# Performance work log

Hardware: AMD Instinct MI355X
Metric: run time of the kernel (lower is better)

Reference implementation:

```python
import jax, jax.numpy as jnp
import numpy as np


def setup_inputs() -> dict:
    key = jax.random.key(0)
    k1, k2, k3, k4, k5 = jax.random.split(key, 5)
    T, R, K, D = 8, 512, 4, 4096          # tiles, rows/tile, group size, in_features
    N_CW = 16384                           # codebook size
    N_TOK = 512                            # tokens
    x = jax.random.normal(k1, (N_TOK, D), dtype=jnp.float32)
    codewords = jax.random.normal(k2, (N_CW, D), dtype=jnp.float32) * 0.02
    indices = jax.random.randint(k3, (T, R, K), 0, N_CW, dtype=jnp.int64)
    rotations = jax.random.normal(k4, (T, D, D), dtype=jnp.float32) * (1.0 / np.sqrt(D))
    scales = jax.random.uniform(k5, (T,), dtype=jnp.float32) + 0.5
    bias = jnp.zeros((D,), dtype=jnp.float32)
    return {"x": x, "codewords": codewords, "indices": indices,
            "rotations": rotations, "scales": scales, "bias": bias}


def reference(x, codewords, indices, rotations, scales, bias):
    # Decode weight tiles: gather [T,R,K,D] -> mean over group -> [T,R,D]
    decoded = codewords[indices].mean(axis=2)
    # Per-tile rotation and scale: [T,R,D] @ [T,D,D] -> [T,R,D]
    decoded = jnp.einsum('trd,tde->tre', decoded, rotations) * scales[:, None, None]
    T, R, D = decoded.shape
    weight = decoded.reshape(T * R, D)     # [out_features, in_features]
    # Linear: x @ W^T + b
    return x @ weight.T + bias
```

## Files before the change

### kernel.cpp

```cpp
#include <hip/hip_runtime.h>

typedef unsigned int uint32;
typedef unsigned short u16;
typedef float fx4 __attribute__((ext_vector_type(4)));
typedef uint32 u32x4 __attribute__((ext_vector_type(4)));

typedef const __attribute__((address_space(1))) void gvoid;
typedef __attribute__((address_space(3))) void lvoid;

#define MFMA_BF16_16x16x32(acc, a, b) \
  asm("v_mfma_f32_16x16x32_bf16 %0, %1, %2, %0" : "+v"(acc) : "v"(a), "v"(b))

#define WAIT_LGKM0() asm volatile("s_waitcnt lgkmcnt(0)" ::: "memory")
#define WAIT_LGKM4() asm volatile("s_waitcnt lgkmcnt(4)" ::: "memory")
#define WAIT_VM0()   asm volatile("s_waitcnt vmcnt(0)" ::: "memory")
#define WAIT_VM3()   asm volatile("s_waitcnt vmcnt(3)" ::: "memory")
#define WAIT_VM6()   asm volatile("s_waitcnt vmcnt(6)" ::: "memory")
#define SFENCE()     __builtin_amdgcn_sched_barrier(0)
#define BARRIER()    do { __builtin_amdgcn_s_barrier(); asm volatile("" ::: "memory"); } while (0)
#define NOWAIT()     do { } while (0)

__device__ __forceinline__ u16 f2bf_rne(float f) {
  uint32 u = __builtin_bit_cast(uint32, f);
  u += 0x7FFFu + ((u >> 16) & 1u);
  return (u16)(u >> 16);
}

__global__ __launch_bounds__(256) void cvtx_kernel(const float* __restrict__ x,
                                                   u16* __restrict__ xb) {
  const int i = blockIdx.x * 256 + threadIdx.x;
  float4 v = ((const float4*)x)[i];
  ushort4 o;
  o.x = f2bf_rne(v.x);
  o.y = f2bf_rne(v.y);
  o.z = f2bf_rne(v.z);
  o.w = f2bf_rne(v.w);
  ((ushort4*)xb)[i] = o;
}

__global__ __launch_bounds__(256) void decode_kernel(
    const float* __restrict__ cw, const int* __restrict__ indices,
    const float* __restrict__ scales, u16* __restrict__ dec) {
  const int row = blockIdx.x;
  const int t = row >> 9;
  const int* ip = indices + (size_t)row * 4;
  const float* c0 = cw + (size_t)ip[0] * 4096;
  const float* c1 = cw + (size_t)ip[1] * 4096;
  const float* c2 = cw + (size_t)ip[2] * 4096;
  const float* c3 = cw + (size_t)ip[3] * 4096;
  const float s = scales[t] * 0.25f;
  u16* orow = dec + (size_t)row * 4096;
  const int tid = threadIdx.x;
#pragma unroll
  for (int j = 0; j < 4; ++j) {
    const int d = j * 1024 + tid * 4;
    float4 a = *(const float4*)(c0 + d);
    float4 b = *(const float4*)(c1 + d);
    float4 c = *(const float4*)(c2 + d);
    float4 e = *(const float4*)(c3 + d);
    ushort4 o;
    o.x = f2bf_rne((a.x + b.x + c.x + e.x) * s);
    o.y = f2bf_rne((a.y + b.y + c.y + e.y) * s);
    o.z = f2bf_rne((a.z + b.z + c.z + e.z) * s);
    o.w = f2bf_rne((a.w + b.w + c.w + e.w) * s);
    *(ushort4*)(orow + d) = o;
  }
}

__global__ __launch_bounds__(512, 2) void gemm_z_kernel(
    const u16* __restrict__ Xb,
    const float* __restrict__ rot,
    u16* __restrict__ Z) {
  __shared__ char sA[49152];
  __shared__ char sB[98304];

  const int lb = blockIdx.x;
  const int swz = ((lb & 7) << 5) | (lb >> 3);
  const int t = swz >> 5;
  const int rem = swz & 31;
  const int nb = rem >> 1, mb = rem & 1;
  const float* Bt = rot + ((size_t)t << 24);
  u16* Ct = Z + ((size_t)t << 21);
  const int aRow0 = mb << 8, bCol0 = nb << 8;
  const int tid = threadIdx.x;
  const int wv = tid >> 6, ln = tid & 63;
  const int lr = ln & 15, lk = ln >> 4;
  const int wr = wv >> 2, wc = wv & 3;

  fx4 acc[8][4] = {};

  const u16* Asrc = Xb + (size_t)(aRow0 + (tid >> 2)) * 4096 +
                    (((tid & 3) ^ ((tid >> 3) & 3)) << 3);
  const float* Bsrc = Bt + (size_t)(bCol0 + (tid >> 3)) * 4096 +
                      (((tid & 7) ^ ((tid >> 3) & 7)) << 2);
  const int gr = (lr >> 1) & 3;
  const int aof = (wr * 128 + lr) * 64 + ((lk ^ gr) << 4);
  const int brx = lr & 7;
  const int c0 = ((2 * lk) ^ brx) << 4;
  const int bof = (wc * 64 + lr) * 128;

#define STAGE_A2(DB, KT)                                                      \
  _Pragma("unroll")                                                           \
  for (int c = 0; c < 2; ++c)                                                 \
    __builtin_amdgcn_global_load_lds(                                         \
        (gvoid*)(Asrc + (size_t)(c * 128) * 4096 + (KT) * 32),                \
        (lvoid*)(sA + (DB) * 16384 + c * 8192 + tid * 16), 16, 0, 0)

#define STAGE_B4(DB, KT)                                                      \
  _Pragma("unroll")                                                           \
  for (int c = 0; c < 4; ++c)                                                 \
    __builtin_amdgcn_global_load_lds(                                         \
        (gvoid*)(Bsrc + (size_t)(c * 64) * 4096 + (KT) * 32),                 \
        (lvoid*)(sB + (DB) * 32768 + c * 8192 + tid * 16), 16, 0, 0)

#define MFMA_HALF(MB)                                                         \
  do {                                                                        \
    __builtin_amdgcn_s_setprio(1);                                            \
    _Pragma("unroll")                                                         \
    for (int m = 0; m < 4; ++m)                                               \
      _Pragma("unroll")                                                       \
      for (int n = 0; n < 4; ++n)                                             \
        MFMA_BF16_16x16x32(acc[(MB) + m][n], af[(MB) + m], bf[n]);            \
    __builtin_amdgcn_s_setprio(0);                                            \
  } while (0)

#define ITER_Z(D, SD, KT, DOSTAGE, TAILW)                                     \
  do {                                                                        \
    const char* pA_ = sA + (D) * 16384;                                       \
    const char* pB_ = sB + (D) * 32768;                                       \
    af[0] = *(const u32x4*)(pA_ + aof);                                       \
    af[1] = *(const u32x4*)(pA_ + aof + 1024);                                \
    af[2] = *(const u32x4*)(pA_ + aof + 2048);                                \
    af[3] = *(const u32x4*)(pA_ + aof + 3072);                                \
    SFENCE();                                                                 \
    ub[0][0] = *(const u32x4*)(pB_ + bof + c0);                               \
    ub[0][1] = *(const u32x4*)(pB_ + bof + (c0 ^ 16));                        \
    ub[1][0] = *(const u32x4*)(pB_ + bof + 2048 + c0);                        \
    ub[1][1] = *(const u32x4*)(pB_ + bof + 2048 + (c0 ^ 16));                 \
    ub[2][0] = *(const u32x4*)(pB_ + bof + 4096 + c0);                        \
    ub[2][1] = *(const u32x4*)(pB_ + bof + 4096 + (c0 ^ 16));                 \
    ub[3][0] = *(const u32x4*)(pB_ + bof + 6144 + c0);                        \
    ub[3][1] = *(const u32x4*)(pB_ + bof + 6144 + (c0 ^ 16));                 \
    SFENCE();                                                                 \
    af[4] = *(const u32x4*)(pA_ + aof + 4096);                                \
    af[5] = *(const u32x4*)(pA_ + aof + 5120);                                \
    af[6] = *(const u32x4*)(pA_ + aof + 6144);                                \
    af[7] = *(const u32x4*)(pA_ + aof + 7168);                                \
    SFENCE();                                                                 \
    if (DOSTAGE) {                                                            \
      STAGE_A2(SD, (KT) + 2);                                                 \
      STAGE_B4(SD, (KT) + 2);                                                 \
    }                                                                         \
    SFENCE();                                                                 \
    WAIT_LGKM4();                               \
    SFENCE();                                                                 \
    _Pragma("unroll")                                                         \
    for (int n = 0; n < 4; ++n) {                                             \
      bf[n][0] = __builtin_amdgcn_perm(ub[n][0][1], ub[n][0][0], 0x07060302u);\
      bf[n][1] = __builtin_amdgcn_perm(ub[n][0][3], ub[n][0][2], 0x07060302u);\
      bf[n][2] = __builtin_amdgcn_perm(ub[n][1][1], ub[n][1][0], 0x07060302u);\
      bf[n][3] = __builtin_amdgcn_perm(ub[n][1][3], ub[n][1][2], 0x07060302u);\
    }                                                                         \
    MFMA_HALF(0);                                                             \
    WAIT_LGKM0();                                                             \
    SFENCE();                                                                 \
    MFMA_HALF(4);                                                             \
    TAILW;                                                                    \
    BARRIER();                                                                \
  } while (0)

  u32x4 af[8], bf[4], ub[4][2];

  STAGE_A2(0, 0);
  STAGE_B4(0, 0);
  SFENCE();
  STAGE_A2(1, 1);
  STAGE_B4(1, 1);
  SFENCE();
  WAIT_VM6();
  BARRIER();

#pragma unroll 1
  for (int kt = 0; kt < 126; kt += 3) {
    ITER_Z(0, 2, kt, 1, WAIT_VM6());
    ITER_Z(1, 0, kt + 1, 1, WAIT_VM6());
    ITER_Z(2, 1, kt + 2, 1, WAIT_VM6());
  }
  ITER_Z(0, 0, 126, 0, WAIT_VM0());
  ITER_Z(1, 0, 127, 0, NOWAIT());

#pragma unroll
  for (int m = 0; m < 8; ++m) {
    const int r0 = aRow0 + wr * 128 + m * 16 + lk * 4;
#pragma unroll
    for (int n = 0; n < 4; ++n) {
      const int col = bCol0 + wc * 64 + n * 16 + lr;
#pragma unroll
      for (int j = 0; j < 4; ++j)
        Ct[(size_t)(r0 + j) * 4096 + col] = f2bf_rne(acc[m][n][j]);
    }
  }
#undef STAGE_A2
#undef STAGE_B4
#undef MFMA_HALF
#undef ITER_Z
}

__global__ __launch_bounds__(256, 2) void gemm_out_kernel(
    const u16* __restrict__ Z,
    const u16* __restrict__ Dec,
    const float* __restrict__ bias,
    float* __restrict__ out) {
  __shared__ char sm[49152];
  const int lb = blockIdx.x;
  const int swz = ((lb & 7) << 5) | (lb >> 3);
  const int t = swz >> 5;
  const int rem = swz & 31;
  const int nb = rem >> 2, mb = rem & 3;
  const u16* At = Z + ((size_t)t << 21);
  const u16* Bt = Dec + ((size_t)t << 21);
  const int aRow0 = mb << 7, bCol0 = nb << 6;
  const int tid = threadIdx.x;
  const int wv = tid >> 6, ln = tid & 63;
  const int lr = ln & 15, lk = ln >> 4;
  const int wr = wv >> 1, wc = wv & 1;

  fx4 acc[4][2] = {};

  const int kswz = (((tid & 3) ^ ((tid >> 3) & 3)) << 3);
  const u16* Asrc = At + (size_t)(aRow0 + (tid >> 2)) * 4096 + kswz;
  const u16* Bsrc = Bt + (size_t)(bCol0 + (tid >> 2)) * 4096 + kswz;
  const int gr = (lr >> 1) & 3;
  const int aof = (wr * 64 + lr) * 64 + ((lk ^ gr) << 4);
  const int bof = 8192 + (wc * 32 + lr) * 64 + ((lk ^ gr) << 4);

#define STAGE_O(buf, kofs)                                                   \
  do {                                                                       \
    _Pragma("unroll")                                                        \
    for (int c = 0; c < 2; ++c)                                              \
      __builtin_amdgcn_global_load_lds(                                      \
          (gvoid*)(Asrc + (size_t)(c << 6) * 4096 + (kofs)),                 \
          (lvoid*)((buf) + c * 4096 + tid * 16), 16, 0, 0);                  \
    __builtin_amdgcn_global_load_lds((gvoid*)(Bsrc + (kofs)),                \
                                     (lvoid*)((buf) + 8192 + tid * 16), 16,  \
                                     0, 0);                                  \
  } while (0)

  char* b0 = sm;
  char* b1 = sm + 12288;
  char* b2 = sm + 24576;
  char* b3 = sm + 36864;
  STAGE_O(b0, 0);
  STAGE_O(b1, 32);
  STAGE_O(b2, 64);
  WAIT_VM6();
  BARRIER();

#pragma unroll 1
  for (int kt = 0; kt < 128; ++kt) {
    if (kt + 3 < 128) STAGE_O(b3, (kt + 3) << 5);
    u32x4 af[4], bf[2];
#pragma unroll
    for (int m = 0; m < 4; ++m)
      af[m] = *(const u32x4*)(b0 + aof + m * 1024);
#pragma unroll
    for (int n = 0; n < 2; ++n)
      bf[n] = *(const u32x4*)(b0 + bof + n * 1024);
    WAIT_LGKM0();
    SFENCE();
#pragma unroll
    for (int m = 0; m < 4; ++m)
#pragma unroll
      for (int n = 0; n < 2; ++n)
        MFMA_BF16_16x16x32(acc[m][n], af[m], bf[n]);
    if (kt + 3 < 128) {
      WAIT_VM6();
    } else if (kt + 2 < 128) {
      WAIT_VM3();
    } else {
      WAIT_VM0();
    }
    BARRIER();
    char* tmp = b0; b0 = b1; b1 = b2; b2 = b3; b3 = tmp;
  }

#pragma unroll
  for (int n = 0; n < 2; ++n) {
    const int colg = (t << 9) + bCol0 + wc * 32 + n * 16 + lr;
    const float bv = bias[colg];
#pragma unroll
    for (int m = 0; m < 4; ++m) {
      const int r0 = aRow0 + wr * 64 + m * 16 + lk * 4;
#pragma unroll
      for (int j = 0; j < 4; ++j)
        out[(size_t)(r0 + j) * 4096 + colg] = acc[m][n][j] + bv;
    }
  }
#undef STAGE_O
}

extern "C" void kernel_launch(void* const* d_in, const int* in_sizes, int n_in,
                              void* d_out, int out_size, void* d_ws, size_t ws_size,
                              hipStream_t stream) {
  const float* x       = (const float*)d_in[0];
  const float* cw      = (const float*)d_in[1];
  const int*   indices = (const int*)d_in[2];
  const float* rot     = (const float*)d_in[3];
  const float* scales  = (const float*)d_in[4];
  const float* bias    = (const float*)d_in[5];
  float* out = (float*)d_out;
  char* ws = (char*)d_ws;

  u16* xb  = (u16*)(ws);
  u16* dec = (u16*)(ws + ((size_t)4 << 20));
  u16* z   = (u16*)(ws + ((size_t)36 << 20));

  decode_kernel<<<dim3(4096), dim3(256), 0, stream>>>(cw, indices, scales, dec);
  cvtx_kernel<<<dim3(2048), dim3(256), 0, stream>>>(x, xb);
  gemm_z_kernel<<<dim3(256), dim3(512), 0, stream>>>(xb, rot, z);
  gemm_out_kernel<<<dim3(256), dim3(256), 0, stream>>>(z, dec, bias, out);
}
```

Measured before the change: 280.0 us.

## Reshape Z-GEMM block tile to cover all 512 rows with narrower columns

Changes the rotation GEMM block tile from 256x256 to 512 rows by 128 columns, so each block covers all tokens and reads each fp32 rotation column slice only once. This halves the redundant global reads of the large fp32 rotation matrix, at the cost of re-reading the small bf16 activations more often. The LDS split between A and B buffers is swapped to match, and the wave layout changes from 2x4 to 4x2.

```diff
diff --git a/kernel.cpp b/kernel.cpp
--- a/kernel.cpp
+++ b/kernel.cpp
@@ -71,47 +71,45 @@
     const u16* __restrict__ Xb,
     const float* __restrict__ rot,
     u16* __restrict__ Z) {
-  __shared__ char sA[49152];
-  __shared__ char sB[98304];
+  __shared__ char sA[98304];
+  __shared__ char sB[49152];
 
   const int lb = blockIdx.x;
   const int swz = ((lb & 7) << 5) | (lb >> 3);
   const int t = swz >> 5;
-  const int rem = swz & 31;
-  const int nb = rem >> 1, mb = rem & 1;
+  const int nb = swz & 31;
   const float* Bt = rot + ((size_t)t << 24);
   u16* Ct = Z + ((size_t)t << 21);
-  const int aRow0 = mb << 8, bCol0 = nb << 8;
+  const int bCol0 = nb << 7;
   const int tid = threadIdx.x;
   const int wv = tid >> 6, ln = tid & 63;
   const int lr = ln & 15, lk = ln >> 4;
-  const int wr = wv >> 2, wc = wv & 3;
+  const int wr = wv >> 1, wc = wv & 1;
 
   fx4 acc[8][4] = {};
 
-  const u16* Asrc = Xb + (size_t)(aRow0 + (tid >> 2)) * 4096 +
+  const u16* Asrc = Xb + (size_t)(tid >> 2) * 4096 +
                     (((tid & 3) ^ ((tid >> 3) & 3)) << 3);
   const float* Bsrc = Bt + (size_t)(bCol0 + (tid >> 3)) * 4096 +
                       (((tid & 7) ^ ((tid >> 3) & 7)) << 2);
   const int gr = (lr >> 1) & 3;
   const int aof = (wr * 128 + lr) * 64 + ((lk ^ gr) << 4);
-  const int brx = lr & 7;
-  const int c0 = ((2 * lk) ^ brx) << 4;
+  const int c0 = ((2 * lk) ^ (lr & 7)) << 4;
   const int bof = (wc * 64 + lr) * 128;
 
-#define STAGE_A2(DB, KT)                                                      \
+#define STAGE_A4(DB, KT)                                                      \
+  _Pragma("unroll")                                                           \
+  for (int c = 0; c < 4; ++c)                                                 \
+    __builtin_amdgcn_global_load_lds(                                         \
+        (gvoid*)(Asrc + (size_t)(c * 128) * 4096 + (KT) * 32),                \
+        (lvoid*)(sA + (DB) * 32768 + c * 8192 + tid * 16), 16, 0, 0)
+
+#define STAGE_B2(DB, KT)                                                      \
   _Pragma("unroll")                                                           \
   for (int c = 0; c < 2; ++c)                                                 \
     __builtin_amdgcn_global_load_lds(                                         \
-        (gvoid*)(Asrc + (size_t)(c * 128) * 4096 + (KT) * 32),                \
-        (lvoid*)(sA + (DB) * 16384 + c * 8192 + tid * 16), 16, 0, 0)
-
-#define STAGE_B4(DB, KT)                                                      \
-  _Pragma("unroll")                                                           \
-  for (int c = 0; c < 4; ++c)                                                 \
-    __builtin_amdgcn_global_load_lds(                                         \
         (gvoid*)(Bsrc + (size_t)(c * 64) * 4096 + (KT) * 32),                 \
-        (lvoid*)(sB + (DB) * 32768 + c * 8192 + tid * 16), 16, 0, 0)
+        (lvoid*)(sB + (DB) * 16384 + c * 8192 + tid * 16), 16, 0, 0)
 
 #define MFMA_HALF(MB)                                                         \
   do {                                                                        \
@@ -126,8 +124,8 @@
 
 #define ITER_Z(D, SD, KT, DOSTAGE, TAILW)                                     \
   do {                                                                        \
-    const char* pA_ = sA + (D) * 16384;                                       \
-    const char* pB_ = sB + (D) * 32768;                                       \
+    const char* pA_ = sA + (D) * 32768;                                       \
+    const char* pB_ = sB + (D) * 16384;                                       \
     af[0] = *(const u32x4*)(pA_ + aof);                                       \
     af[1] = *(const u32x4*)(pA_ + aof + 1024);                                \
     af[2] = *(const u32x4*)(pA_ + aof + 2048);                                \
@@ -148,8 +146,8 @@
     af[7] = *(const u32x4*)(pA_ + aof + 7168);                                \
     SFENCE();                                                                 \
     if (DOSTAGE) {                                                            \
-      STAGE_A2(SD, (KT) + 2);                                                 \
-      STAGE_B4(SD, (KT) + 2);                                                 \
+      STAGE_A4(SD, (KT) + 2);                                                 \
+      STAGE_B2(SD, (KT) + 2);                                                 \
     }                                                                         \
     SFENCE();                                                                 \
     WAIT_LGKM4();                               \
@@ -171,11 +169,11 @@
 
   u32x4 af[8], bf[4], ub[4][2];
 
-  STAGE_A2(0, 0);
-  STAGE_B4(0, 0);
+  STAGE_A4(0, 0);
+  STAGE_B2(0, 0);
   SFENCE();
-  STAGE_A2(1, 1);
-  STAGE_B4(1, 1);
+  STAGE_A4(1, 1);
+  STAGE_B2(1, 1);
   SFENCE();
   WAIT_VM6();
   BARRIER();
@@ -191,7 +189,7 @@
 
 #pragma unroll
   for (int m = 0; m < 8; ++m) {
-    const int r0 = aRow0 + wr * 128 + m * 16 + lk * 4;
+    const int r0 = wr * 128 + m * 16 + lk * 4;
 #pragma unroll
     for (int n = 0; n < 4; ++n) {
       const int col = bCol0 + wc * 64 + n * 16 + lr;
@@ -200,8 +198,8 @@
         Ct[(size_t)(r0 + j) * 4096 + col] = f2bf_rne(acc[m][n][j]);
     }
   }
-#undef STAGE_A2
-#undef STAGE_B4
+#undef STAGE_A4
+#undef STAGE_B2
 #undef MFMA_HALF
 #undef ITER_Z
 }
```

Result: no change. 285.5 us (+1.9%).

## Fuse codeword decode into Z GEMM launch and shrink GEMM tiles

Applied to the files above, without the earlier changes.

Merges the decode kernel into the Z-GEMM launch: the first 256 blocks decode 16 rows each while the remaining 1024 blocks compute 128x128 tiles of X·R. The GEMM moves from 256x256 tiles with 512 threads and a triple-buffered pipeline to 128x128 tiles with 256 threads, double buffering and a full vmcnt(0) wait each iteration. The intent is to overlap memory-bound decode with the GEMM, cut one launch, and raise occupancy with more blocks. The cost is lower data reuse per tile, more global traffic for the fp32 rotation matrix, and a shallower prefetch pipeline.

```diff
diff --git a/kernel.cpp b/kernel.cpp
--- a/kernel.cpp
+++ b/kernel.cpp
@@ -12,7 +12,6 @@
   asm("v_mfma_f32_16x16x32_bf16 %0, %1, %2, %0" : "+v"(acc) : "v"(a), "v"(b))
 
 #define WAIT_LGKM0() asm volatile("s_waitcnt lgkmcnt(0)" ::: "memory")
-#define WAIT_LGKM4() asm volatile("s_waitcnt lgkmcnt(4)" ::: "memory")
 #define WAIT_VM0()   asm volatile("s_waitcnt vmcnt(0)" ::: "memory")
 #define WAIT_VM3()   asm volatile("s_waitcnt vmcnt(3)" ::: "memory")
 #define WAIT_VM6()   asm volatile("s_waitcnt vmcnt(6)" ::: "memory")
@@ -38,101 +37,98 @@
   ((ushort4*)xb)[i] = o;
 }
 
-__global__ __launch_bounds__(256) void decode_kernel(
+__device__ __forceinline__ void decode_body(
+    int bid, const float* __restrict__ cw, const int* __restrict__ indices,
+    const float* __restrict__ scales, u16* __restrict__ dec) {
+  const int tid = threadIdx.x;
+#pragma unroll 1
+  for (int rr = 0; rr < 16; ++rr) {
+    const int row = bid * 16 + rr;
+    const int t = row >> 9;
+    const int* ip = indices + (size_t)row * 4;
+    const float* c0 = cw + (size_t)ip[0] * 4096;
+    const float* c1 = cw + (size_t)ip[1] * 4096;
+    const float* c2 = cw + (size_t)ip[2] * 4096;
+    const float* c3 = cw + (size_t)ip[3] * 4096;
+    const float s = scales[t] * 0.25f;
+    u16* orow = dec + (size_t)row * 4096;
+#pragma unroll
+    for (int j = 0; j < 4; ++j) {
+      const int d = j * 1024 + tid * 4;
+      float4 a = *(const float4*)(c0 + d);
+      float4 b = *(const float4*)(c1 + d);
+      float4 c = *(const float4*)(c2 + d);
+      float4 e = *(const float4*)(c3 + d);
+      ushort4 o;
+      o.x = f2bf_rne((a.x + b.x + c.x + e.x) * s);
+      o.y = f2bf_rne((a.y + b.y + c.y + e.y) * s);
+      o.z = f2bf_rne((a.z + b.z + c.z + e.z) * s);
+      o.w = f2bf_rne((a.w + b.w + c.w + e.w) * s);
+      *(ushort4*)(orow + d) = o;
+    }
+  }
+}
+
+__global__ __launch_bounds__(256, 3) void fused_z_decode_kernel(
+    const u16* __restrict__ Xb,
+    const float* __restrict__ rot,
+    u16* __restrict__ Z,
     const float* __restrict__ cw, const int* __restrict__ indices,
     const float* __restrict__ scales, u16* __restrict__ dec) {
-  const int row = blockIdx.x;
-  const int t = row >> 9;
-  const int* ip = indices + (size_t)row * 4;
-  const float* c0 = cw + (size_t)ip[0] * 4096;
-  const float* c1 = cw + (size_t)ip[1] * 4096;
-  const float* c2 = cw + (size_t)ip[2] * 4096;
-  const float* c3 = cw + (size_t)ip[3] * 4096;
-  const float s = scales[t] * 0.25f;
-  u16* orow = dec + (size_t)row * 4096;
-  const int tid = threadIdx.x;
-#pragma unroll
-  for (int j = 0; j < 4; ++j) {
-    const int d = j * 1024 + tid * 4;
-    float4 a = *(const float4*)(c0 + d);
-    float4 b = *(const float4*)(c1 + d);
-    float4 c = *(const float4*)(c2 + d);
-    float4 e = *(const float4*)(c3 + d);
-    ushort4 o;
-    o.x = f2bf_rne((a.x + b.x + c.x + e.x) * s);
-    o.y = f2bf_rne((a.y + b.y + c.y + e.y) * s);
-    o.z = f2bf_rne((a.z + b.z + c.z + e.z) * s);
-    o.w = f2bf_rne((a.w + b.w + c.w + e.w) * s);
-    *(ushort4*)(orow + d) = o;
-  }
-}
-
-__global__ __launch_bounds__(512, 2) void gemm_z_kernel(
-    const u16* __restrict__ Xb,
-    const float* __restrict__ rot,
-    u16* __restrict__ Z) {
-  __shared__ char sA[49152];
-  __shared__ char sB[98304];
-
-  const int lb = blockIdx.x;
-  const int swz = ((lb & 7) << 5) | (lb >> 3);
-  const int t = swz >> 5;
-  const int rem = swz & 31;
-  const int nb = rem >> 1, mb = rem & 1;
+  __shared__ char sA[16384];
+  __shared__ char sB[32768];
+
+  const int bid = blockIdx.x;
+  if (bid < 256) {
+    decode_body(bid, cw, indices, scales, dec);
+    return;
+  }
+  const int lb = bid - 256;
+  const int swz = ((lb & 7) << 7) | (lb >> 3);
+  const int t = swz >> 7;
+  const int rem = swz & 127;
+  const int nb = rem >> 2, mb = rem & 3;
   const float* Bt = rot + ((size_t)t << 24);
   u16* Ct = Z + ((size_t)t << 21);
-  const int aRow0 = mb << 8, bCol0 = nb << 8;
+  const int aRow0 = mb << 7, bCol0 = nb << 7;
   const int tid = threadIdx.x;
   const int wv = tid >> 6, ln = tid & 63;
   const int lr = ln & 15, lk = ln >> 4;
-  const int wr = wv >> 2, wc = wv & 3;
-
-  fx4 acc[8][4] = {};
+  const int wr = wv >> 1, wc = wv & 1;
+
+  fx4 acc[4][4] = {};
 
   const u16* Asrc = Xb + (size_t)(aRow0 + (tid >> 2)) * 4096 +
                     (((tid & 3) ^ ((tid >> 3) & 3)) << 3);
   const float* Bsrc = Bt + (size_t)(bCol0 + (tid >> 3)) * 4096 +
                       (((tid & 7) ^ ((tid >> 3) & 7)) << 2);
   const int gr = (lr >> 1) & 3;
-  const int aof = (wr * 128 + lr) * 64 + ((lk ^ gr) << 4);
-  const int brx = lr & 7;
-  const int c0 = ((2 * lk) ^ brx) << 4;
+  const int aof = (wr * 64 + lr) * 64 + ((lk ^ gr) << 4);
+  const int c0 = ((2 * lk) ^ (lr & 7)) << 4;
   const int bof = (wc * 64 + lr) * 128;
 
 #define STAGE_A2(DB, KT)                                                      \
   _Pragma("unroll")                                                           \
   for (int c = 0; c < 2; ++c)                                                 \
     __builtin_amdgcn_global_load_lds(                                         \
-        (gvoid*)(Asrc + (size_t)(c * 128) * 4096 + (KT) * 32),                \
-        (lvoid*)(sA + (DB) * 16384 + c * 8192 + tid * 16), 16, 0, 0)
+        (gvoid*)(Asrc + (size_t)(c * 64) * 4096 + (KT) * 32),                 \
+        (lvoid*)(sA + (DB) * 8192 + c * 4096 + tid * 16), 16, 0, 0)
 
 #define STAGE_B4(DB, KT)                                                      \
   _Pragma("unroll")                                                           \
   for (int c = 0; c < 4; ++c)                                                 \
     __builtin_amdgcn_global_load_lds(                                         \
-        (gvoid*)(Bsrc + (size_t)(c * 64) * 4096 + (KT) * 32),                 \
-        (lvoid*)(sB + (DB) * 32768 + c * 8192 + tid * 16), 16, 0, 0)
-
-#define MFMA_HALF(MB)                                                         \
+        (gvoid*)(Bsrc + (size_t)(c * 32) * 4096 + (KT) * 32),                 \
+        (lvoid*)(sB + (DB) * 16384 + c * 4096 + tid * 16), 16, 0, 0)
+
+#define ITER_Z(D, KT, DOSTAGE, TAILW)                                         \
   do {                                                                        \
-    __builtin_amdgcn_s_setprio(1);                                            \
-    _Pragma("unroll")                                                         \
-    for (int m = 0; m < 4; ++m)                                               \
-      _Pragma("unroll")                                                       \
-      for (int n = 0; n < 4; ++n)                                             \
-        MFMA_BF16_16x16x32(acc[(MB) + m][n], af[(MB) + m], bf[n]);            \
-    __builtin_amdgcn_s_setprio(0);                                            \
-  } while (0)
-
-#define ITER_Z(D, SD, KT, DOSTAGE, TAILW)                                     \
-  do {                                                                        \
-    const char* pA_ = sA + (D) * 16384;                                       \
-    const char* pB_ = sB + (D) * 32768;                                       \
+    const char* pA_ = sA + (D) * 8192;                                        \
+    const char* pB_ = sB + (D) * 16384;                                       \
     af[0] = *(const u32x4*)(pA_ + aof);                                       \
     af[1] = *(const u32x4*)(pA_ + aof + 1024);                                \
     af[2] = *(const u32x4*)(pA_ + aof + 2048);                                \
     af[3] = *(const u32x4*)(pA_ + aof + 3072);                                \
-    SFENCE();                                                                 \
     ub[0][0] = *(const u32x4*)(pB_ + bof + c0);                               \
     ub[0][1] = *(const u32x4*)(pB_ + bof + (c0 ^ 16));                        \
     ub[1][0] = *(const u32x4*)(pB_ + bof + 2048 + c0);                        \
@@ -142,17 +138,9 @@
     ub[3][0] = *(const u32x4*)(pB_ + bof + 6144 + c0);                        \
     ub[3][1] = *(const u32x4*)(pB_ + bof + 6144 + (c0 ^ 16));                 \
     SFENCE();                                                                 \
-    af[4] = *(const u32x4*)(pA_ + aof + 4096);                                \
-    af[5] = *(const u32x4*)(pA_ + aof + 5120);                                \
-    af[6] = *(const u32x4*)(pA_ + aof + 6144);                                \
-    af[7] = *(const u32x4*)(pA_ + aof + 7168);                                \
+    if (DOSTAGE) { STAGE_A2((D) ^ 1, (KT) + 1); STAGE_B4((D) ^ 1, (KT) + 1); }\
     SFENCE();                                                                 \
-    if (DOSTAGE) {                                                            \
-      STAGE_A2(SD, (KT) + 2);                                                 \
-      STAGE_B4(SD, (KT) + 2);                                                 \
-    }                                                                         \
-    SFENCE();                                                                 \
-    WAIT_LGKM4();                               \
+    WAIT_LGKM0();                                                             \
     SFENCE();                                                                 \
     _Pragma("unroll")                                                         \
     for (int n = 0; n < 4; ++n) {                                             \
@@ -161,37 +149,36 @@
       bf[n][2] = __builtin_amdgcn_perm(ub[n][1][1], ub[n][1][0], 0x07060302u);\
       bf[n][3] = __builtin_amdgcn_perm(ub[n][1][3], ub[n][1][2], 0x07060302u);\
     }                                                                         \
-    MFMA_HALF(0);                                                             \
-    WAIT_LGKM0();                                                             \
-    SFENCE();                                                                 \
-    MFMA_HALF(4);                                                             \
+    __builtin_amdgcn_s_setprio(1);                                            \
+    _Pragma("unroll")                                                         \
+    for (int m = 0; m < 4; ++m)                                               \
+      _Pragma("unroll")                                                       \
+      for (int n = 0; n < 4; ++n)                                             \
+        MFMA_BF16_16x16x32(acc[m][n], af[m], bf[n]);                          \
+    __builtin_amdgcn_s_setprio(0);                                            \
     TAILW;                                                                    \
     BARRIER();                                                                \
   } while (0)
 
-  u32x4 af[8], bf[4], ub[4][2];
+  u32x4 af[4], bf[4], ub[4][2];
 
   STAGE_A2(0, 0);
   STAGE_B4(0, 0);
   SFENCE();
-  STAGE_A2(1, 1);
-  STAGE_B4(1, 1);
-  SFENCE();
-  WAIT_VM6();
+  WAIT_VM0();
   BARRIER();
 
 #pragma unroll 1
-  for (int kt = 0; kt < 126; kt += 3) {
-    ITER_Z(0, 2, kt, 1, WAIT_VM6());
-    ITER_Z(1, 0, kt + 1, 1, WAIT_VM6());
-    ITER_Z(2, 1, kt + 2, 1, WAIT_VM6());
-  }
-  ITER_Z(0, 0, 126, 0, WAIT_VM0());
-  ITER_Z(1, 0, 127, 0, NOWAIT());
-
-#pragma unroll
-  for (int m = 0; m < 8; ++m) {
-    const int r0 = aRow0 + wr * 128 + m * 16 + lk * 4;
+  for (int kt2 = 0; kt2 < 126; kt2 += 2) {
+    ITER_Z(0, kt2, 1, WAIT_VM0());
+    ITER_Z(1, kt2 + 1, 1, WAIT_VM0());
+  }
+  ITER_Z(0, 126, 1, WAIT_VM0());
+  ITER_Z(1, 127, 0, NOWAIT());
+
+#pragma unroll
+  for (int m = 0; m < 4; ++m) {
+    const int r0 = aRow0 + wr * 64 + m * 16 + lk * 4;
 #pragma unroll
     for (int n = 0; n < 4; ++n) {
       const int col = bCol0 + wc * 64 + n * 16 + lr;
@@ -202,7 +189,6 @@
   }
 #undef STAGE_A2
 #undef STAGE_B4
-#undef MFMA_HALF
 #undef ITER_Z
 }
 
@@ -315,8 +301,8 @@
   u16* dec = (u16*)(ws + ((size_t)4 << 20));
   u16* z   = (u16*)(ws + ((size_t)36 << 20));
 
-  decode_kernel<<<dim3(4096), dim3(256), 0, stream>>>(cw, indices, scales, dec);
   cvtx_kernel<<<dim3(2048), dim3(256), 0, stream>>>(x, xb);
-  gemm_z_kernel<<<dim3(256), dim3(512), 0, stream>>>(xb, rot, z);
+  fused_z_decode_kernel<<<dim3(1280), dim3(256), 0, stream>>>(
+      xb, rot, z, cw, indices, scales, dec);
   gemm_out_kernel<<<dim3(256), dim3(256), 0, stream>>>(z, dec, bias, out);
 }
```

Result: slower. 353.5 us (+26.2%).
